# Optimization experiments

Measured on AMD Instinct MI355X. Metric: run time of the kernel, lower is better.

## Reference

```python
import jax, jax.numpy as jnp
import numpy as np

NUM_HEADS = 32
NUM_KV_HEADS = 8
HEAD_DIM = 128
SEQ = 2048
MASK_BLOCK = 128  # diffusion-LM denoising block size


def setup_inputs() -> dict:
    key = jax.random.key(0)
    kq, kk, kv = jax.random.split(key, 3)
    q = jax.random.normal(kq, (SEQ, NUM_HEADS * HEAD_DIM), dtype=jnp.float32)
    k = jax.random.normal(kk, (SEQ, NUM_KV_HEADS * HEAD_DIM), dtype=jnp.float32)
    v = jax.random.normal(kv, (SEQ, NUM_KV_HEADS * HEAD_DIM), dtype=jnp.float32)
    # block-causal mask at MASK_BLOCK granularity: token_q attends to token_kv
    # iff block(token_kv) <= block(token_q). Every row has >=1 True entry.
    blk = jnp.arange(SEQ) // MASK_BLOCK
    block_mask = blk[None, :] <= blk[:, None]  # [S, S] bool
    return {"q": q, "k": k, "v": v, "block_mask": block_mask}


def reference(q, k, v, block_mask):
    S = q.shape[0]
    scale = 1.0 / np.sqrt(HEAD_DIM).astype(np.float32)  # flex_attention default scale
    qh = q.reshape(S, NUM_HEADS, HEAD_DIM)       # [S, Hq, D]
    kh = k.reshape(S, NUM_KV_HEADS, HEAD_DIM)    # [S, Hkv, D]
    vh = v.reshape(S, NUM_KV_HEADS, HEAD_DIM)
    # GQA: repeat each kv head over its query-head group
    group = NUM_HEADS // NUM_KV_HEADS
    kh = jnp.repeat(kh, group, axis=1)           # [S, Hq, D]
    vh = jnp.repeat(vh, group, axis=1)
    scores = jnp.einsum('qhd,khd->hqk', qh, kh) * scale  # [Hq, S, S]
    neg_inf = jnp.finfo(scores.dtype).min
    scores = jnp.where(block_mask[None, :, :], scores, neg_inf)
    probs = jax.nn.softmax(scores, axis=-1)
    o = jnp.einsum('hqk,khd->qhd', probs, vh)    # [S, Hq, D]
    return o.reshape(S, NUM_HEADS * HEAD_DIM)
```

## Files before the change

### kernel.cpp

```cpp
#include <hip/hip_runtime.h>
#include <hip/hip_bf16.h>

#define SEQL  2048
#define NHQ   32
#define NHKV  8
#define HD    128

typedef __attribute__((ext_vector_type(4))) float          f32x4;
typedef __attribute__((ext_vector_type(8))) short          bf16x8;
typedef __attribute__((ext_vector_type(4))) unsigned short u16x4;
typedef __attribute__((ext_vector_type(8))) unsigned short u16x8;

__device__ __forceinline__ unsigned short f2bf(float f) {
  union { float f; unsigned u; } v; v.f = f;
  unsigned u = v.u;
  return (unsigned short)((u + 0x7fffu + ((u >> 16) & 1u)) >> 16);
}

__device__ __forceinline__ unsigned cvtpk_bf16(float lo, float hi) {
  unsigned r;
  asm("v_cvt_pk_bf16_f32 %0, %1, %2" : "=v"(r) : "v"(lo), "v"(hi));
  return r;
}

__device__ __forceinline__ void gload16(const void* g, void* l) {
  __builtin_amdgcn_global_load_lds(
      (const __attribute__((address_space(1))) unsigned int*)g,
      (__attribute__((address_space(3))) unsigned int*)l, 16, 0, 0);
}

__global__ __launch_bounds__(256) void prep_k(const float* __restrict__ k,
                                              unsigned short* __restrict__ kws) {
  int t = blockIdx.x * 256 + threadIdx.x;
  int s   = t >> 7;
  int col = (t & 127) << 3;
  int hkv = col >> 7;
  int d0  = col & 127;
  const float* src = k + (size_t)s * (NHKV * HD) + col;
  f32x4 a = *(const f32x4*)src;
  f32x4 b = *(const f32x4*)(src + 4);
  u16x8 r;
  r[0] = f2bf(a[0]); r[1] = f2bf(a[1]); r[2] = f2bf(a[2]); r[3] = f2bf(a[3]);
  r[4] = f2bf(b[0]); r[5] = f2bf(b[1]); r[6] = f2bf(b[2]); r[7] = f2bf(b[3]);
  int tile = s >> 6, rr = s & 63;
  int idx = (rr * 128 + d0) ^ ((rr & 7) << 3);
  *(u16x8*)(kws + (((size_t)(hkv * 32 + tile)) << 13) + idx) = r;
}

__global__ __launch_bounds__(256) void prep_v(const float* __restrict__ v,
                                              unsigned short* __restrict__ vws) {
  int t = blockIdx.x * 256 + threadIdx.x;
  int d    = t & 127;
  int hkv  = (t >> 7) & 7;
  int rest = t >> 10;
  int tile = rest >> 3;
  int g    = (rest >> 2) & 1;
  int lhi  = rest & 3;
  int s0   = tile * 64 + g * 32 + lhi * 4;
  const float* src = v + (size_t)s0 * (NHKV * HD) + hkv * HD + d;
  u16x8 r;
  #pragma unroll
  for (int j = 0; j < 8; ++j) {
    int soff = ((j >> 2) << 4) + (j & 3);
    r[j] = f2bf(src[(size_t)soff * (NHKV * HD)]);
  }
  int idx = (d * 64 + g * 32 + lhi * 8) ^ ((d & 7) << 3);
  *(u16x8*)(vws + (((size_t)(hkv * 32 + tile)) << 13) + idx) = r;
}

__global__ __launch_bounds__(256, 2) void attn_fwd12(
    const float* __restrict__ q,
    const unsigned short* __restrict__ kws,
    const unsigned short* __restrict__ vws,
    float* __restrict__ out)
{
  __shared__ unsigned short Kb[2][8192];
  __shared__ unsigned short Vb[2][8192];

  const int tid  = threadIdx.x;
  const int lane = tid & 63;
  const int wv   = tid >> 6;
  const int l15  = lane & 15;
  const int lhi  = lane >> 4;
  const int swzK = (l15 & 7) << 3;

  const int bx   = blockIdx.x;
  const int hkv  = bx & 7;
  const int h    = hkv * 4 + ((bx >> 3) & 3);
  const int idx2 = bx >> 5;
  const int pr   = (idx2 < 8) ? idx2 : (23 - idx2);
  const int qtA  = pr, qtB = 31 - pr;
  const int nA   = ((qtA >> 1) + 1) * 2;
  const int nB   = 34 - nA;

  const float qscale = 0.08838834764831845f * 1.4426950408889634f;
  const float THR = 11.5f;

  const unsigned short* ktiles = kws + (((size_t)hkv * 32) << 13);
  const unsigned short* vtiles = vws + (((size_t)hkv * 32) << 13);

  bf16x8 qfA[4], qfB[4];
  f32x4 oaccA[8], oaccB[8];
  float mrunA = -1e30f, lrunA = 0.f, mrunB = -1e30f, lrunB = 0.f;

  {
    const float* qbase = q + (size_t)(qtA * 64 + wv * 16 + l15) * (NHQ * HD) + h * HD + lhi * 8;
    #pragma unroll
    for (int c = 0; c < 4; ++c) {
      f32x4 a = *(const f32x4*)(qbase + c * 32);
      f32x4 b = *(const f32x4*)(qbase + c * 32 + 4);
      bf16x8 r;
      r[0] = (short)f2bf(a[0] * qscale);
      r[1] = (short)f2bf(a[1] * qscale);
      r[2] = (short)f2bf(a[2] * qscale);
      r[3] = (short)f2bf(a[3] * qscale);
      r[4] = (short)f2bf(b[0] * qscale);
      r[5] = (short)f2bf(b[1] * qscale);
      r[6] = (short)f2bf(b[2] * qscale);
      r[7] = (short)f2bf(b[3] * qscale);
      qfA[c] = r;
    }
  }
  {
    const float* qbase = q + (size_t)(qtB * 64 + wv * 16 + l15) * (NHQ * HD) + h * HD + lhi * 8;
    #pragma unroll
    for (int c = 0; c < 4; ++c) {
      f32x4 a = *(const f32x4*)(qbase + c * 32);
      f32x4 b = *(const f32x4*)(qbase + c * 32 + 4);
      bf16x8 r;
      r[0] = (short)f2bf(a[0] * qscale);
      r[1] = (short)f2bf(a[1] * qscale);
      r[2] = (short)f2bf(a[2] * qscale);
      r[3] = (short)f2bf(a[3] * qscale);
      r[4] = (short)f2bf(b[0] * qscale);
      r[5] = (short)f2bf(b[1] * qscale);
      r[6] = (short)f2bf(b[2] * qscale);
      r[7] = (short)f2bf(b[3] * qscale);
      qfB[c] = r;
    }
  }
  #pragma unroll
  for (int i = 0; i < 8; ++i) {
    oaccA[i] = (f32x4){0.f, 0.f, 0.f, 0.f};
    oaccB[i] = (f32x4){0.f, 0.f, 0.f, 0.f};
  }

  auto STAGE = [&](int b, int kvt) {
    const char* gk = (const char*)(ktiles + ((size_t)kvt << 13));
    const char* gv = (const char*)(vtiles + ((size_t)kvt << 13));
    char* lk = (char*)&Kb[b][0];
    char* lv = (char*)&Vb[b][0];
    #pragma unroll
    for (int i = 0; i < 4; ++i) {
      const int off = wv * 4096 + i * 1024;
      gload16(gk + off + lane * 16, lk + off);
      gload16(gv + off + lane * 16, lv + off);
    }
  };

  auto computeDual = [&](int b) {
    f32x4 saA[4], saB[4];
    __builtin_amdgcn_s_setprio(1);
    #pragma unroll
    for (int sub = 0; sub < 4; ++sub) {
      f32x4 aA = (f32x4){0.f, 0.f, 0.f, 0.f};
      f32x4 aB = (f32x4){0.f, 0.f, 0.f, 0.f};
      const int row = sub * 16 + l15;
      #pragma unroll
      for (int c = 0; c < 4; ++c) {
        bf16x8 kf = *(const bf16x8*)(&Kb[b][(row * 128 + c * 32 + lhi * 8) ^ swzK]);
        aA = __builtin_amdgcn_mfma_f32_16x16x32_bf16(kf, qfA[c], aA, 0, 0, 0);
        aB = __builtin_amdgcn_mfma_f32_16x16x32_bf16(kf, qfB[c], aB, 0, 0, 0);
      }
      saA[sub] = aA; saB[sub] = aB;
    }
    __builtin_amdgcn_s_setprio(0);
    float a0 = fmaxf(fmaxf(saA[0][0], saA[0][1]), fmaxf(saA[0][2], saA[0][3]));
    float a1 = fmaxf(fmaxf(saA[1][0], saA[1][1]), fmaxf(saA[1][2], saA[1][3]));
    float a2 = fmaxf(fmaxf(saA[2][0], saA[2][1]), fmaxf(saA[2][2], saA[2][3]));
    float a3 = fmaxf(fmaxf(saA[3][0], saA[3][1]), fmaxf(saA[3][2], saA[3][3]));
    float mtA = fmaxf(fmaxf(a0, a1), fmaxf(a2, a3));
    float b0 = fmaxf(fmaxf(saB[0][0], saB[0][1]), fmaxf(saB[0][2], saB[0][3]));
    float b1 = fmaxf(fmaxf(saB[1][0], saB[1][1]), fmaxf(saB[1][2], saB[1][3]));
    float b2 = fmaxf(fmaxf(saB[2][0], saB[2][1]), fmaxf(saB[2][2], saB[2][3]));
    float b3 = fmaxf(fmaxf(saB[3][0], saB[3][1]), fmaxf(saB[3][2], saB[3][3]));
    float mtB = fmaxf(fmaxf(b0, b1), fmaxf(b2, b3));
    mtA = fmaxf(mtA, __shfl_xor(mtA, 16));
    mtA = fmaxf(mtA, __shfl_xor(mtA, 32));
    mtB = fmaxf(mtB, __shfl_xor(mtB, 16));
    mtB = fmaxf(mtB, __shfl_xor(mtB, 32));
    int need = (mtA > mrunA + THR) || (mtB > mrunB + THR);
    if (__any(need)) {
      float mnA = fmaxf(mrunA, mtA), mnB = fmaxf(mrunB, mtB);
      float cA = exp2f(mrunA - mnA), cB = exp2f(mrunB - mnB);
      mrunA = mnA; mrunB = mnB;
      lrunA *= cA; lrunB *= cB;
      #pragma unroll
      for (int d = 0; d < 8; ++d) { oaccA[d] *= cA; oaccB[d] *= cB; }
    }
    unsigned pwA[8], pwB[8];
    {
      float ts = 0.f;
      #pragma unroll
      for (int sub = 0; sub < 4; ++sub) {
        float p0 = exp2f(saA[sub][0] - mrunA);
        float p1 = exp2f(saA[sub][1] - mrunA);
        float p2 = exp2f(saA[sub][2] - mrunA);
        float p3 = exp2f(saA[sub][3] - mrunA);
        ts += (p0 + p1) + (p2 + p3);
        pwA[2 * sub]     = cvtpk_bf16(p0, p1);
        pwA[2 * sub + 1] = cvtpk_bf16(p2, p3);
      }
      ts += __shfl_xor(ts, 16);
      ts += __shfl_xor(ts, 32);
      lrunA += ts;
    }
    {
      float ts = 0.f;
      #pragma unroll
      for (int sub = 0; sub < 4; ++sub) {
        float p0 = exp2f(saB[sub][0] - mrunB);
        float p1 = exp2f(saB[sub][1] - mrunB);
        float p2 = exp2f(saB[sub][2] - mrunB);
        float p3 = exp2f(saB[sub][3] - mrunB);
        ts += (p0 + p1) + (p2 + p3);
        pwB[2 * sub]     = cvtpk_bf16(p0, p1);
        pwB[2 * sub + 1] = cvtpk_bf16(p2, p3);
      }
      ts += __shfl_xor(ts, 16);
      ts += __shfl_xor(ts, 32);
      lrunB += ts;
    }
    __builtin_amdgcn_s_setprio(1);
    #pragma unroll
    for (int kc = 0; kc < 2; ++kc) {
      bf16x8 vr[8];
      #pragma unroll
      for (int dsub = 0; dsub < 8; ++dsub) {
        const int d = dsub * 16 + l15;
        vr[dsub] = *(const bf16x8*)(&Vb[b][(d * 64 + kc * 32 + lhi * 8) ^ swzK]);
      }
      union { unsigned u[4]; bf16x8 v8; } pA, pB;
      pA.u[0] = pwA[4 * kc + 0]; pA.u[1] = pwA[4 * kc + 1];
      pA.u[2] = pwA[4 * kc + 2]; pA.u[3] = pwA[4 * kc + 3];
      pB.u[0] = pwB[4 * kc + 0]; pB.u[1] = pwB[4 * kc + 1];
      pB.u[2] = pwB[4 * kc + 2]; pB.u[3] = pwB[4 * kc + 3];
      bf16x8 pfA = pA.v8, pfB = pB.v8;
      #pragma unroll
      for (int dsub = 0; dsub < 8; ++dsub) {
        oaccA[dsub] = __builtin_amdgcn_mfma_f32_16x16x32_bf16(vr[dsub], pfA, oaccA[dsub], 0, 0, 0);
        oaccB[dsub] = __builtin_amdgcn_mfma_f32_16x16x32_bf16(vr[dsub], pfB, oaccB[dsub], 0, 0, 0);
      }
    }
    __builtin_amdgcn_s_setprio(0);
  };

  auto computeB = [&](int b) {
    f32x4 sa[4];
    __builtin_amdgcn_s_setprio(1);
    #pragma unroll
    for (int sub = 0; sub < 4; ++sub) {
      f32x4 acc = (f32x4){0.f, 0.f, 0.f, 0.f};
      const int row = sub * 16 + l15;
      #pragma unroll
      for (int c = 0; c < 4; ++c) {
        bf16x8 kf = *(const bf16x8*)(&Kb[b][(row * 128 + c * 32 + lhi * 8) ^ swzK]);
        acc = __builtin_amdgcn_mfma_f32_16x16x32_bf16(kf, qfB[c], acc, 0, 0, 0);
      }
      sa[sub] = acc;
    }
    __builtin_amdgcn_s_setprio(0);
    bf16x8 vr[2][8];
    #pragma unroll
    for (int kc = 0; kc < 2; ++kc)
      #pragma unroll
      for (int dsub = 0; dsub < 8; ++dsub) {
        const int d = dsub * 16 + l15;
        vr[kc][dsub] = *(const bf16x8*)(&Vb[b][(d * 64 + kc * 32 + lhi * 8) ^ swzK]);
      }
    float m0 = fmaxf(fmaxf(sa[0][0], sa[0][1]), fmaxf(sa[0][2], sa[0][3]));
    float m1 = fmaxf(fmaxf(sa[1][0], sa[1][1]), fmaxf(sa[1][2], sa[1][3]));
    float m2 = fmaxf(fmaxf(sa[2][0], sa[2][1]), fmaxf(sa[2][2], sa[2][3]));
    float m3 = fmaxf(fmaxf(sa[3][0], sa[3][1]), fmaxf(sa[3][2], sa[3][3]));
    float mt = fmaxf(fmaxf(m0, m1), fmaxf(m2, m3));
    mt = fmaxf(mt, __shfl_xor(mt, 16));
    mt = fmaxf(mt, __shfl_xor(mt, 32));
    if (__any(mt > mrunB + THR)) {
      float mn = fmaxf(mrunB, mt);
      float c0 = exp2f(mrunB - mn);
      mrunB = mn; lrunB *= c0;
      #pragma unroll
      for (int d = 0; d < 8; ++d) oaccB[d] *= c0;
    }
    unsigned pw[8];
    {
      float ts = 0.f;
      #pragma unroll
      for (int sub = 0; sub < 4; ++sub) {
        float p0 = exp2f(sa[sub][0] - mrunB);
        float p1 = exp2f(sa[sub][1] - mrunB);
        float p2 = exp2f(sa[sub][2] - mrunB);
        float p3 = exp2f(sa[sub][3] - mrunB);
        ts += (p0 + p1) + (p2 + p3);
        pw[2 * sub]     = cvtpk_bf16(p0, p1);
        pw[2 * sub + 1] = cvtpk_bf16(p2, p3);
      }
      ts += __shfl_xor(ts, 16);
      ts += __shfl_xor(ts, 32);
      lrunB += ts;
    }
    __builtin_amdgcn_s_setprio(1);
    #pragma unroll
    for (int kc = 0; kc < 2; ++kc) {
      union { unsigned u[4]; bf16x8 v8; } pk;
      pk.u[0] = pw[4 * kc + 0];
      pk.u[1] = pw[4 * kc + 1];
      pk.u[2] = pw[4 * kc + 2];
      pk.u[3] = pw[4 * kc + 3];
      bf16x8 pf = pk.v8;
      #pragma unroll
      for (int dsub = 0; dsub < 8; ++dsub) {
        oaccB[dsub] = __builtin_amdgcn_mfma_f32_16x16x32_bf16(vr[kc][dsub], pf, oaccB[dsub], 0, 0, 0);
      }
    }
    __builtin_amdgcn_s_setprio(0);
  };

  STAGE(0, 0);
  int buf = 0;
  #pragma unroll 1
  for (int t = 0; t < nB; ++t) {
    if (t == nA) {
      float invl = 1.0f / lrunA;
      float* ob = out + (size_t)(qtA * 64 + wv * 16 + l15) * (NHQ * HD) + h * HD + lhi * 4;
      #pragma unroll
      for (int dsub = 0; dsub < 8; ++dsub)
        *(f32x4*)(ob + dsub * 16) = oaccA[dsub] * invl;
    }
    if (t + 1 < nB) {
      STAGE(buf ^ 1, t + 1);
      asm volatile("s_waitcnt vmcnt(8)" ::: "memory");
    } else {
      asm volatile("s_waitcnt vmcnt(0)" ::: "memory");
    }
    __builtin_amdgcn_s_barrier();
    asm volatile("" ::: "memory");
    if (t < nA) computeDual(buf);
    else        computeB(buf);
    asm volatile("" ::: "memory");
    __builtin_amdgcn_s_barrier();
    buf ^= 1;
  }
  {
    float invl = 1.0f / lrunB;
    float* ob = out + (size_t)(qtB * 64 + wv * 16 + l15) * (NHQ * HD) + h * HD + lhi * 4;
    #pragma unroll
    for (int dsub = 0; dsub < 8; ++dsub)
      *(f32x4*)(ob + dsub * 16) = oaccB[dsub] * invl;
  }
}

__global__ __launch_bounds__(256) void attn_v1(
    const float* __restrict__ q,
    const float* __restrict__ k,
    const float* __restrict__ v,
    float* __restrict__ out)
{
  __shared__ unsigned short Ks[64 * 128];
  __shared__ unsigned short Vt[128 * 64];
  __shared__ unsigned short Psl[4][16 * 64];

  const int tid  = threadIdx.x;
  const int lane = tid & 63;
  const int wv   = tid >> 6;
  const int bx   = blockIdx.x;
  const int h    = bx & 31;
  const int qt   = (SEQL / 64 - 1) - (bx >> 5);
  const int q0   = qt * 64;
  const int hkv  = h >> 2;
  const int l15 = lane & 15;
  const int lhi = lane >> 4;
  const float qscale = 0.08838834764831845f * 1.4426950408889634f;

  bf16x8 qf[4];
  {
    const float* qbase = q + (size_t)(q0 + wv * 16 + l15) * (NHQ * HD) + h * HD + lhi * 8;
    #pragma unroll
    for (int c = 0; c < 4; ++c) {
      const float* p8 = qbase + c * 32;
      f32x4 a = *(const f32x4*)p8;
      f32x4 b = *(const f32x4*)(p8 + 4);
      bf16x8 r;
      r[0] = (short)f2bf(a[0] * qscale); r[1] = (short)f2bf(a[1] * qscale);
      r[2] = (short)f2bf(a[2] * qscale); r[3] = (short)f2bf(a[3] * qscale);
      r[4] = (short)f2bf(b[0] * qscale); r[5] = (short)f2bf(b[1] * qscale);
      r[6] = (short)f2bf(b[2] * qscale); r[7] = (short)f2bf(b[3] * qscale);
      qf[c] = r;
    }
  }
  f32x4 oacc[8];
  #pragma unroll
  for (int i = 0; i < 8; ++i) oacc[i] = (f32x4){0.f, 0.f, 0.f, 0.f};
  float mrun[4], lrun[4];
  #pragma unroll
  for (int r = 0; r < 4; ++r) { mrun[r] = -1e30f; lrun[r] = 0.f; }
  const int ntiles = ((q0 >> 7) + 1) * 2;
  for (int t = 0; t < ntiles; ++t) {
    const int kv0 = t * 64;
    __syncthreads();
    #pragma unroll
    for (int it = 0; it < 8; ++it) {
      int c = it * 256 + tid;
      int row = c >> 5;
      int dc = (c & 31) << 2;
      f32x4 x = *(const f32x4*)(k + (size_t)(kv0 + row) * (NHKV * HD) + hkv * HD + dc);
      u16x4 y;
      y[0] = f2bf(x[0]); y[1] = f2bf(x[1]); y[2] = f2bf(x[2]); y[3] = f2bf(x[3]);
      int idx = (row * HD + dc) ^ ((row & 7) << 3);
      *(u16x4*)(&Ks[idx]) = y;
    }
    {
      int row = tid >> 2;
      int db = (tid & 3) << 5;
      const float* vbase = v + (size_t)(kv0 + row) * (NHKV * HD) + hkv * HD + db;
      #pragma unroll
      for (int it = 0; it < 8; ++it) {
        f32x4 x = *(const f32x4*)(vbase + it * 4);
        int d0 = db + it * 4;
        #pragma unroll
        for (int j = 0; j < 4; ++j) {
          int d = d0 + j;
          int idx = (d * 64 + row) ^ ((d & 7) << 3);
          Vt[idx] = f2bf(x[j]);
        }
      }
    }
    __syncthreads();
    f32x4 sacc[4];
    #pragma unroll
    for (int sub = 0; sub < 4; ++sub) {
      f32x4 acc = (f32x4){0.f, 0.f, 0.f, 0.f};
      #pragma unroll
      for (int c = 0; c < 4; ++c) {
        int row = sub * 16 + l15;
        int idx = (row * HD + c * 32 + lhi * 8) ^ ((row & 7) << 3);
        bf16x8 kf = *(const bf16x8*)(&Ks[idx]);
        acc = __builtin_amdgcn_mfma_f32_16x16x32_bf16(qf[c], kf, acc, 0, 0, 0);
      }
      sacc[sub] = acc;
    }
    float corr[4];
    #pragma unroll
    for (int r = 0; r < 4; ++r) {
      float mt = fmaxf(fmaxf(sacc[0][r], sacc[1][r]), fmaxf(sacc[2][r], sacc[3][r]));
      #pragma unroll
      for (int off = 1; off < 16; off <<= 1) mt = fmaxf(mt, __shfl_xor(mt, off));
      float mnew = fmaxf(mrun[r], mt);
      corr[r] = exp2f(mrun[r] - mnew);
      mrun[r] = mnew;
      float p0 = exp2f(sacc[0][r] - mnew);
      float p1 = exp2f(sacc[1][r] - mnew);
      float p2 = exp2f(sacc[2][r] - mnew);
      float p3 = exp2f(sacc[3][r] - mnew);
      int qr = (lhi << 2) + r;
      int swz = (qr & 7) << 3;
      int bq = qr * 64;
      Psl[wv][(bq + 0  + l15) ^ swz] = f2bf(p0);
      Psl[wv][(bq + 16 + l15) ^ swz] = f2bf(p1);
      Psl[wv][(bq + 32 + l15) ^ swz] = f2bf(p2);
      Psl[wv][(bq + 48 + l15) ^ swz] = f2bf(p3);
      float ts = p0 + p1 + p2 + p3;
      #pragma unroll
      for (int off = 1; off < 16; off <<= 1) ts += __shfl_xor(ts, off);
      lrun[r] = lrun[r] * corr[r] + ts;
    }
    #pragma unroll
    for (int dsub = 0; dsub < 8; ++dsub) {
      f32x4 o = oacc[dsub];
      o[0] *= corr[0]; o[1] *= corr[1]; o[2] *= corr[2]; o[3] *= corr[3];
      oacc[dsub] = o;
    }
    #pragma unroll
    for (int kc = 0; kc < 2; ++kc) {
      int pidx = (l15 * 64 + kc * 32 + lhi * 8) ^ ((l15 & 7) << 3);
      bf16x8 pf = *(const bf16x8*)(&Psl[wv][pidx]);
      #pragma unroll
      for (int dsub = 0; dsub < 8; ++dsub) {
        int d = dsub * 16 + l15;
        int vidx = (d * 64 + kc * 32 + lhi * 8) ^ ((d & 7) << 3);
        bf16x8 vf = *(const bf16x8*)(&Vt[vidx]);
        oacc[dsub] = __builtin_amdgcn_mfma_f32_16x16x32_bf16(pf, vf, oacc[dsub], 0, 0, 0);
      }
    }
  }
  float inv[4];
  #pragma unroll
  for (int r = 0; r < 4; ++r) inv[r] = 1.0f / lrun[r];
  float* obase = out + (size_t)(q0 + wv * 16 + (lhi << 2)) * (NHQ * HD) + h * HD + l15;
  #pragma unroll
  for (int dsub = 0; dsub < 8; ++dsub) {
    #pragma unroll
    for (int r = 0; r < 4; ++r) {
      obase[(size_t)r * (NHQ * HD) + dsub * 16] = oacc[dsub][r] * inv[r];
    }
  }
}

extern "C" void kernel_launch(void* const* d_in, const int* in_sizes, int n_in,
                              void* d_out, int out_size, void* d_ws, size_t ws_size,
                              hipStream_t stream) {
  const float* q = (const float*)d_in[0];
  const float* k = (const float*)d_in[1];
  const float* v = (const float*)d_in[2];
  float* out = (float*)d_out;
  const size_t prepNeed = (size_t)8 * 1024 * 1024 + 512;
  if (ws_size >= prepNeed) {
    unsigned short* kws = (unsigned short*)d_ws;
    unsigned short* vws = kws + (size_t)4 * 1024 * 1024 / 2;
    prep_k<<<1024, 256, 0, stream>>>(k, kws);
    prep_v<<<1024, 256, 0, stream>>>(v, vws);
    attn_fwd12<<<512, 256, 0, stream>>>(q, kws, vws, out);
  } else {
    attn_v1<<<1024, 256, 0, stream>>>(q, k, v, out);
  }
}
```

Measured before the change: 101.5 us.

## Split dual/single-tile attention loops and stream V fragments to cut register pressure

Splits the main loop into a dual-tile phase (tiles A and B together) and a B-only phase, removing the per-iteration branch and writing out A's result between the two loops. In the dual phase, the PV products for A and B are done one after the other, and V fragments are loaded from LDS inside the MFMA loop instead of holding 8 V registers and both P vectors at once. It also drops the minBlocks=2 launch bound. The aim is lower VGPR pressure and simpler control flow, at the cost of reading V from LDS twice per tile in the dual phase and possibly a different occupancy.

```diff
diff --git a/kernel.cpp b/kernel.cpp
--- a/kernel.cpp
+++ b/kernel.cpp
@@ -68,7 +68,7 @@
   *(u16x8*)(vws + (((size_t)(hkv * 32 + tile)) << 13) + idx) = r;
 }
 
-__global__ __launch_bounds__(256, 2) void attn_fwd12(
+__global__ __launch_bounds__(256) void attn_fwd13(
     const float* __restrict__ q,
     const unsigned short* __restrict__ kws,
     const unsigned short* __restrict__ vws,
@@ -99,12 +99,21 @@
   const unsigned short* ktiles = kws + (((size_t)hkv * 32) << 13);
   const unsigned short* vtiles = vws + (((size_t)hkv * 32) << 13);
 
-  bf16x8 qfA[4], qfB[4];
-  f32x4 oaccA[8], oaccB[8];
-  float mrunA = -1e30f, lrunA = 0.f, mrunB = -1e30f, lrunB = 0.f;
-
-  {
-    const float* qbase = q + (size_t)(qtA * 64 + wv * 16 + l15) * (NHQ * HD) + h * HD + lhi * 8;
+  auto STAGE = [&](int b, int kvt) {
+    const char* gk = (const char*)(ktiles + ((size_t)kvt << 13));
+    const char* gv = (const char*)(vtiles + ((size_t)kvt << 13));
+    char* lk = (char*)&Kb[b][0];
+    char* lv = (char*)&Vb[b][0];
+    #pragma unroll
+    for (int i = 0; i < 4; ++i) {
+      const int off = wv * 4096 + i * 1024;
+      gload16(gk + off + lane * 16, lk + off);
+      gload16(gv + off + lane * 16, lv + off);
+    }
+  };
+
+  auto loadQf = [&](int qt, bf16x8* qf) {
+    const float* qbase = q + (size_t)(qt * 64 + wv * 16 + l15) * (NHQ * HD) + h * HD + lhi * 8;
     #pragma unroll
     for (int c = 0; c < 4; ++c) {
       f32x4 a = *(const f32x4*)(qbase + c * 32);
@@ -118,225 +127,152 @@
       r[5] = (short)f2bf(b[1] * qscale);
       r[6] = (short)f2bf(b[2] * qscale);
       r[7] = (short)f2bf(b[3] * qscale);
-      qfA[c] = r;
-    }
-  }
-  {
-    const float* qbase = q + (size_t)(qtB * 64 + wv * 16 + l15) * (NHQ * HD) + h * HD + lhi * 8;
-    #pragma unroll
-    for (int c = 0; c < 4; ++c) {
-      f32x4 a = *(const f32x4*)(qbase + c * 32);
-      f32x4 b = *(const f32x4*)(qbase + c * 32 + 4);
-      bf16x8 r;
-      r[0] = (short)f2bf(a[0] * qscale);
-      r[1] = (short)f2bf(a[1] * qscale);
-      r[2] = (short)f2bf(a[2] * qscale);
-      r[3] = (short)f2bf(a[3] * qscale);
-      r[4] = (short)f2bf(b[0] * qscale);
-      r[5] = (short)f2bf(b[1] * qscale);
-      r[6] = (short)f2bf(b[2] * qscale);
-      r[7] = (short)f2bf(b[3] * qscale);
-      qfB[c] = r;
-    }
-  }
+      qf[c] = r;
+    }
+  };
+
+  bf16x8 qfA[4], qfB[4];
+  loadQf(qtA, qfA);
+  loadQf(qtB, qfB);
+
+  f32x4 oaccA[8], oaccB[8];
   #pragma unroll
   for (int i = 0; i < 8; ++i) {
     oaccA[i] = (f32x4){0.f, 0.f, 0.f, 0.f};
     oaccB[i] = (f32x4){0.f, 0.f, 0.f, 0.f};
   }
-
-  auto STAGE = [&](int b, int kvt) {
-    const char* gk = (const char*)(ktiles + ((size_t)kvt << 13));
-    const char* gv = (const char*)(vtiles + ((size_t)kvt << 13));
-    char* lk = (char*)&Kb[b][0];
-    char* lv = (char*)&Vb[b][0];
-    #pragma unroll
-    for (int i = 0; i < 4; ++i) {
-      const int off = wv * 4096 + i * 1024;
-      gload16(gk + off + lane * 16, lk + off);
-      gload16(gv + off + lane * 16, lv + off);
-    }
-  };
-
-  auto computeDual = [&](int b) {
-    f32x4 saA[4], saB[4];
-    __builtin_amdgcn_s_setprio(1);
-    #pragma unroll
-    for (int sub = 0; sub < 4; ++sub) {
-      f32x4 aA = (f32x4){0.f, 0.f, 0.f, 0.f};
-      f32x4 aB = (f32x4){0.f, 0.f, 0.f, 0.f};
-      const int row = sub * 16 + l15;
-      #pragma unroll
-      for (int c = 0; c < 4; ++c) {
-        bf16x8 kf = *(const bf16x8*)(&Kb[b][(row * 128 + c * 32 + lhi * 8) ^ swzK]);
-        aA = __builtin_amdgcn_mfma_f32_16x16x32_bf16(kf, qfA[c], aA, 0, 0, 0);
-        aB = __builtin_amdgcn_mfma_f32_16x16x32_bf16(kf, qfB[c], aB, 0, 0, 0);
-      }
-      saA[sub] = aA; saB[sub] = aB;
-    }
-    __builtin_amdgcn_s_setprio(0);
-    float a0 = fmaxf(fmaxf(saA[0][0], saA[0][1]), fmaxf(saA[0][2], saA[0][3]));
-    float a1 = fmaxf(fmaxf(saA[1][0], saA[1][1]), fmaxf(saA[1][2], saA[1][3]));
-    float a2 = fmaxf(fmaxf(saA[2][0], saA[2][1]), fmaxf(saA[2][2], saA[2][3]));
-    float a3 = fmaxf(fmaxf(saA[3][0], saA[3][1]), fmaxf(saA[3][2], saA[3][3]));
-    float mtA = fmaxf(fmaxf(a0, a1), fmaxf(a2, a3));
-    float b0 = fmaxf(fmaxf(saB[0][0], saB[0][1]), fmaxf(saB[0][2], saB[0][3]));
-    float b1 = fmaxf(fmaxf(saB[1][0], saB[1][1]), fmaxf(saB[1][2], saB[1][3]));
-    float b2 = fmaxf(fmaxf(saB[2][0], saB[2][1]), fmaxf(saB[2][2], saB[2][3]));
-    float b3 = fmaxf(fmaxf(saB[3][0], saB[3][1]), fmaxf(saB[3][2], saB[3][3]));
-    float mtB = fmaxf(fmaxf(b0, b1), fmaxf(b2, b3));
-    mtA = fmaxf(mtA, __shfl_xor(mtA, 16));
-    mtA = fmaxf(mtA, __shfl_xor(mtA, 32));
-    mtB = fmaxf(mtB, __shfl_xor(mtB, 16));
-    mtB = fmaxf(mtB, __shfl_xor(mtB, 32));
-    int need = (mtA > mrunA + THR) || (mtB > mrunB + THR);
-    if (__any(need)) {
-      float mnA = fmaxf(mrunA, mtA), mnB = fmaxf(mrunB, mtB);
-      float cA = exp2f(mrunA - mnA), cB = exp2f(mrunB - mnB);
-      mrunA = mnA; mrunB = mnB;
-      lrunA *= cA; lrunB *= cB;
-      #pragma unroll
-      for (int d = 0; d < 8; ++d) { oaccA[d] *= cA; oaccB[d] *= cB; }
-    }
-    unsigned pwA[8], pwB[8];
-    {
-      float ts = 0.f;
-      #pragma unroll
-      for (int sub = 0; sub < 4; ++sub) {
-        float p0 = exp2f(saA[sub][0] - mrunA);
-        float p1 = exp2f(saA[sub][1] - mrunA);
-        float p2 = exp2f(saA[sub][2] - mrunA);
-        float p3 = exp2f(saA[sub][3] - mrunA);
-        ts += (p0 + p1) + (p2 + p3);
-        pwA[2 * sub]     = cvtpk_bf16(p0, p1);
-        pwA[2 * sub + 1] = cvtpk_bf16(p2, p3);
-      }
-      ts += __shfl_xor(ts, 16);
-      ts += __shfl_xor(ts, 32);
-      lrunA += ts;
-    }
-    {
-      float ts = 0.f;
-      #pragma unroll
-      for (int sub = 0; sub < 4; ++sub) {
-        float p0 = exp2f(saB[sub][0] - mrunB);
-        float p1 = exp2f(saB[sub][1] - mrunB);
-        float p2 = exp2f(saB[sub][2] - mrunB);
-        float p3 = exp2f(saB[sub][3] - mrunB);
-        ts += (p0 + p1) + (p2 + p3);
-        pwB[2 * sub]     = cvtpk_bf16(p0, p1);
-        pwB[2 * sub + 1] = cvtpk_bf16(p2, p3);
-      }
-      ts += __shfl_xor(ts, 16);
-      ts += __shfl_xor(ts, 32);
-      lrunB += ts;
-    }
-    __builtin_amdgcn_s_setprio(1);
-    #pragma unroll
-    for (int kc = 0; kc < 2; ++kc) {
-      bf16x8 vr[8];
-      #pragma unroll
-      for (int dsub = 0; dsub < 8; ++dsub) {
-        const int d = dsub * 16 + l15;
-        vr[dsub] = *(const bf16x8*)(&Vb[b][(d * 64 + kc * 32 + lhi * 8) ^ swzK]);
-      }
-      union { unsigned u[4]; bf16x8 v8; } pA, pB;
-      pA.u[0] = pwA[4 * kc + 0]; pA.u[1] = pwA[4 * kc + 1];
-      pA.u[2] = pwA[4 * kc + 2]; pA.u[3] = pwA[4 * kc + 3];
-      pB.u[0] = pwB[4 * kc + 0]; pB.u[1] = pwB[4 * kc + 1];
-      pB.u[2] = pwB[4 * kc + 2]; pB.u[3] = pwB[4 * kc + 3];
-      bf16x8 pfA = pA.v8, pfB = pB.v8;
-      #pragma unroll
-      for (int dsub = 0; dsub < 8; ++dsub) {
-        oaccA[dsub] = __builtin_amdgcn_mfma_f32_16x16x32_bf16(vr[dsub], pfA, oaccA[dsub], 0, 0, 0);
-        oaccB[dsub] = __builtin_amdgcn_mfma_f32_16x16x32_bf16(vr[dsub], pfB, oaccB[dsub], 0, 0, 0);
-      }
-    }
-    __builtin_amdgcn_s_setprio(0);
-  };
-
-  auto computeB = [&](int b) {
-    f32x4 sa[4];
-    __builtin_amdgcn_s_setprio(1);
-    #pragma unroll
-    for (int sub = 0; sub < 4; ++sub) {
-      f32x4 acc = (f32x4){0.f, 0.f, 0.f, 0.f};
-      const int row = sub * 16 + l15;
-      #pragma unroll
-      for (int c = 0; c < 4; ++c) {
-        bf16x8 kf = *(const bf16x8*)(&Kb[b][(row * 128 + c * 32 + lhi * 8) ^ swzK]);
-        acc = __builtin_amdgcn_mfma_f32_16x16x32_bf16(kf, qfB[c], acc, 0, 0, 0);
-      }
-      sa[sub] = acc;
-    }
-    __builtin_amdgcn_s_setprio(0);
-    bf16x8 vr[2][8];
-    #pragma unroll
-    for (int kc = 0; kc < 2; ++kc)
-      #pragma unroll
-      for (int dsub = 0; dsub < 8; ++dsub) {
-        const int d = dsub * 16 + l15;
-        vr[kc][dsub] = *(const bf16x8*)(&Vb[b][(d * 64 + kc * 32 + lhi * 8) ^ swzK]);
-      }
-    float m0 = fmaxf(fmaxf(sa[0][0], sa[0][1]), fmaxf(sa[0][2], sa[0][3]));
-    float m1 = fmaxf(fmaxf(sa[1][0], sa[1][1]), fmaxf(sa[1][2], sa[1][3]));
-    float m2 = fmaxf(fmaxf(sa[2][0], sa[2][1]), fmaxf(sa[2][2], sa[2][3]));
-    float m3 = fmaxf(fmaxf(sa[3][0], sa[3][1]), fmaxf(sa[3][2], sa[3][3]));
-    float mt = fmaxf(fmaxf(m0, m1), fmaxf(m2, m3));
-    mt = fmaxf(mt, __shfl_xor(mt, 16));
-    mt = fmaxf(mt, __shfl_xor(mt, 32));
-    if (__any(mt > mrunB + THR)) {
-      float mn = fmaxf(mrunB, mt);
-      float c0 = exp2f(mrunB - mn);
-      mrunB = mn; lrunB *= c0;
-      #pragma unroll
-      for (int d = 0; d < 8; ++d) oaccB[d] *= c0;
-    }
-    unsigned pw[8];
-    {
-      float ts = 0.f;
-      #pragma unroll
-      for (int sub = 0; sub < 4; ++sub) {
-        float p0 = exp2f(sa[sub][0] - mrunB);
-        float p1 = exp2f(sa[sub][1] - mrunB);
-        float p2 = exp2f(sa[sub][2] - mrunB);
-        float p3 = exp2f(sa[sub][3] - mrunB);
-        ts += (p0 + p1) + (p2 + p3);
-        pw[2 * sub]     = cvtpk_bf16(p0, p1);
-        pw[2 * sub + 1] = cvtpk_bf16(p2, p3);
-      }
-      ts += __shfl_xor(ts, 16);
-      ts += __shfl_xor(ts, 32);
-      lrunB += ts;
-    }
-    __builtin_amdgcn_s_setprio(1);
-    #pragma unroll
-    for (int kc = 0; kc < 2; ++kc) {
-      union { unsigned u[4]; bf16x8 v8; } pk;
-      pk.u[0] = pw[4 * kc + 0];
-      pk.u[1] = pw[4 * kc + 1];
-      pk.u[2] = pw[4 * kc + 2];
-      pk.u[3] = pw[4 * kc + 3];
-      bf16x8 pf = pk.v8;
-      #pragma unroll
-      for (int dsub = 0; dsub < 8; ++dsub) {
-        oaccB[dsub] = __builtin_amdgcn_mfma_f32_16x16x32_bf16(vr[kc][dsub], pf, oaccB[dsub], 0, 0, 0);
-      }
-    }
-    __builtin_amdgcn_s_setprio(0);
-  };
+  float mrunA = -1e30f, lrunA = 0.f, mrunB = -1e30f, lrunB = 0.f;
 
   STAGE(0, 0);
   int buf = 0;
+
   #pragma unroll 1
-  for (int t = 0; t < nB; ++t) {
-    if (t == nA) {
-      float invl = 1.0f / lrunA;
-      float* ob = out + (size_t)(qtA * 64 + wv * 16 + l15) * (NHQ * HD) + h * HD + lhi * 4;
-      #pragma unroll
-      for (int dsub = 0; dsub < 8; ++dsub)
-        *(f32x4*)(ob + dsub * 16) = oaccA[dsub] * invl;
-    }
+  for (int t = 0; t < nA; ++t) {
+    STAGE(buf ^ 1, t + 1);
+    asm volatile("s_waitcnt vmcnt(8)" ::: "memory");
+    __builtin_amdgcn_s_barrier();
+    asm volatile("" ::: "memory");
+    {
+      const int b = buf;
+      f32x4 saA[4], saB[4];
+      __builtin_amdgcn_s_setprio(1);
+      #pragma unroll
+      for (int sub = 0; sub < 4; ++sub) {
+        f32x4 aA = (f32x4){0.f, 0.f, 0.f, 0.f};
+        f32x4 aB = (f32x4){0.f, 0.f, 0.f, 0.f};
+        const int row = sub * 16 + l15;
+        #pragma unroll
+        for (int c = 0; c < 4; ++c) {
+          bf16x8 kf = *(const bf16x8*)(&Kb[b][(row * 128 + c * 32 + lhi * 8) ^ swzK]);
+          aA = __builtin_amdgcn_mfma_f32_16x16x32_bf16(kf, qfA[c], aA, 0, 0, 0);
+          aB = __builtin_amdgcn_mfma_f32_16x16x32_bf16(kf, qfB[c], aB, 0, 0, 0);
+        }
+        saA[sub] = aA; saB[sub] = aB;
+      }
+      __builtin_amdgcn_s_setprio(0);
+      float a0 = fmaxf(fmaxf(saA[0][0], saA[0][1]), fmaxf(saA[0][2], saA[0][3]));
+      float a1 = fmaxf(fmaxf(saA[1][0], saA[1][1]), fmaxf(saA[1][2], saA[1][3]));
+      float a2 = fmaxf(fmaxf(saA[2][0], saA[2][1]), fmaxf(saA[2][2], saA[2][3]));
+      float a3 = fmaxf(fmaxf(saA[3][0], saA[3][1]), fmaxf(saA[3][2], saA[3][3]));
+      float mtA = fmaxf(fmaxf(a0, a1), fmaxf(a2, a3));
+      float b0 = fmaxf(fmaxf(saB[0][0], saB[0][1]), fmaxf(saB[0][2], saB[0][3]));
+      float b1 = fmaxf(fmaxf(saB[1][0], saB[1][1]), fmaxf(saB[1][2], saB[1][3]));
+      float b2 = fmaxf(fmaxf(saB[2][0], saB[2][1]), fmaxf(saB[2][2], saB[2][3]));
+      float b3 = fmaxf(fmaxf(saB[3][0], saB[3][1]), fmaxf(saB[3][2], saB[3][3]));
+      float mtB = fmaxf(fmaxf(b0, b1), fmaxf(b2, b3));
+      mtA = fmaxf(mtA, __shfl_xor(mtA, 16));
+      mtA = fmaxf(mtA, __shfl_xor(mtA, 32));
+      mtB = fmaxf(mtB, __shfl_xor(mtB, 16));
+      mtB = fmaxf(mtB, __shfl_xor(mtB, 32));
+      int need = (mtA > mrunA + THR) || (mtB > mrunB + THR);
+      if (__any(need)) {
+        float mnA = fmaxf(mrunA, mtA), mnB = fmaxf(mrunB, mtB);
+        float cA = exp2f(mrunA - mnA), cB = exp2f(mrunB - mnB);
+        mrunA = mnA; mrunB = mnB;
+        lrunA *= cA; lrunB *= cB;
+        #pragma unroll
+        for (int d = 0; d < 8; ++d) { oaccA[d] *= cA; oaccB[d] *= cB; }
+      }
+      {
+        unsigned pw[8];
+        float ts = 0.f;
+        #pragma unroll
+        for (int sub = 0; sub < 4; ++sub) {
+          float p0 = exp2f(saA[sub][0] - mrunA);
+          float p1 = exp2f(saA[sub][1] - mrunA);
+          float p2 = exp2f(saA[sub][2] - mrunA);
+          float p3 = exp2f(saA[sub][3] - mrunA);
+          ts += (p0 + p1) + (p2 + p3);
+          pw[2 * sub]     = cvtpk_bf16(p0, p1);
+          pw[2 * sub + 1] = cvtpk_bf16(p2, p3);
+        }
+        ts += __shfl_xor(ts, 16);
+        ts += __shfl_xor(ts, 32);
+        lrunA += ts;
+        __builtin_amdgcn_s_setprio(1);
+        #pragma unroll
+        for (int kc = 0; kc < 2; ++kc) {
+          union { unsigned u[4]; bf16x8 v8; } pk;
+          pk.u[0] = pw[4 * kc + 0]; pk.u[1] = pw[4 * kc + 1];
+          pk.u[2] = pw[4 * kc + 2]; pk.u[3] = pw[4 * kc + 3];
+          bf16x8 pf = pk.v8;
+          #pragma unroll
+          for (int dsub = 0; dsub < 8; ++dsub) {
+            const int d = dsub * 16 + l15;
+            bf16x8 vf = *(const bf16x8*)(&Vb[b][(d * 64 + kc * 32 + lhi * 8) ^ swzK]);
+            oaccA[dsub] = __builtin_amdgcn_mfma_f32_16x16x32_bf16(vf, pf, oaccA[dsub], 0, 0, 0);
+          }
+        }
+        __builtin_amdgcn_s_setprio(0);
+      }
+      {
+        unsigned pw[8];
+        float ts = 0.f;
+        #pragma unroll
+        for (int sub = 0; sub < 4; ++sub) {
+          float p0 = exp2f(saB[sub][0] - mrunB);
+          float p1 = exp2f(saB[sub][1] - mrunB);
+          float p2 = exp2f(saB[sub][2] - mrunB);
+          float p3 = exp2f(saB[sub][3] - mrunB);
+          ts += (p0 + p1) + (p2 + p3);
+          pw[2 * sub]     = cvtpk_bf16(p0, p1);
+          pw[2 * sub + 1] = cvtpk_bf16(p2, p3);
+        }
+        ts += __shfl_xor(ts, 16);
+        ts += __shfl_xor(ts, 32);
+        lrunB += ts;
+        __builtin_amdgcn_s_setprio(1);
+        #pragma unroll
+        for (int kc = 0; kc < 2; ++kc) {
+          union { unsigned u[4]; bf16x8 v8; } pk;
+          pk.u[0] = pw[4 * kc + 0]; pk.u[1] = pw[4 * kc + 1];
+          pk.u[2] = pw[4 * kc + 2]; pk.u[3] = pw[4 * kc + 3];
+          bf16x8 pf = pk.v8;
+          #pragma unroll
+          for (int dsub = 0; dsub < 8; ++dsub) {
+            const int d = dsub * 16 + l15;
+            bf16x8 vf = *(const bf16x8*)(&Vb[b][(d * 64 + kc * 32 + lhi * 8) ^ swzK]);
+            oaccB[dsub] = __builtin_amdgcn_mfma_f32_16x16x32_bf16(vf, pf, oaccB[dsub], 0, 0, 0);
+          }
+        }
+        __builtin_amdgcn_s_setprio(0);
+      }
+    }
+    asm volatile("" ::: "memory");
+    __builtin_amdgcn_s_barrier();
+    buf ^= 1;
+  }
+
+  {
+    float invl = 1.0f / lrunA;
+    float* ob = out + (size_t)(qtA * 64 + wv * 16 + l15) * (NHQ * HD) + h * HD + lhi * 4;
+    #pragma unroll
+    for (int dsub = 0; dsub < 8; ++dsub)
+      *(f32x4*)(ob + dsub * 16) = oaccA[dsub] * invl;
+  }
+
+  #pragma unroll 1
+  for (int t = nA; t < nB; ++t) {
     if (t + 1 < nB) {
       STAGE(buf ^ 1, t + 1);
       asm volatile("s_waitcnt vmcnt(8)" ::: "memory");
@@ -345,12 +281,82 @@
     }
     __builtin_amdgcn_s_barrier();
     asm volatile("" ::: "memory");
-    if (t < nA) computeDual(buf);
-    else        computeB(buf);
+    {
+      const int b = buf;
+      f32x4 sa[4];
+      __builtin_amdgcn_s_setprio(1);
+      #pragma unroll
+      for (int sub = 0; sub < 4; ++sub) {
+        f32x4 acc = (f32x4){0.f, 0.f, 0.f, 0.f};
+        const int row = sub * 16 + l15;
+        #pragma unroll
+        for (int c = 0; c < 4; ++c) {
+          bf16x8 kf = *(const bf16x8*)(&Kb[b][(row * 128 + c * 32 + lhi * 8) ^ swzK]);
+          acc = __builtin_amdgcn_mfma_f32_16x16x32_bf16(kf, qfB[c], acc, 0, 0, 0);
+        }
+        sa[sub] = acc;
+      }
+      __builtin_amdgcn_s_setprio(0);
+      bf16x8 vr[2][8];
+      #pragma unroll
+      for (int kc = 0; kc < 2; ++kc)
+        #pragma unroll
+        for (int dsub = 0; dsub < 8; ++dsub) {
+          const int d = dsub * 16 + l15;
+          vr[kc][dsub] = *(const bf16x8*)(&Vb[b][(d * 64 + kc * 32 + lhi * 8) ^ swzK]);
+        }
+      float m0 = fmaxf(fmaxf(sa[0][0], sa[0][1]), fmaxf(sa[0][2], sa[0][3]));
+      float m1 = fmaxf(fmaxf(sa[1][0], sa[1][1]), fmaxf(sa[1][2], sa[1][3]));
+      float m2 = fmaxf(fmaxf(sa[2][0], sa[2][1]), fmaxf(sa[2][2], sa[2][3]));
+      float m3 = fmaxf(fmaxf(sa[3][0], sa[3][1]), fmaxf(sa[3][2], sa[3][3]));
+      float mt = fmaxf(fmaxf(m0, m1), fmaxf(m2, m3));
+      mt = fmaxf(mt, __shfl_xor(mt, 16));
+      mt = fmaxf(mt, __shfl_xor(mt, 32));
+      if (__any(mt > mrunB + THR)) {
+        float mn = fmaxf(mrunB, mt);
+        float c0 = exp2f(mrunB - mn);
+        mrunB = mn; lrunB *= c0;
+        #pragma unroll
+        for (int d = 0; d < 8; ++d) oaccB[d] *= c0;
+      }
+      unsigned pw[8];
+      {
+        float ts = 0.f;
+        #pragma unroll
+        for (int sub = 0; sub < 4; ++sub) {
+          float p0 = exp2f(sa[sub][0] - mrunB);
+          float p1 = exp2f(sa[sub][1] - mrunB);
+          float p2 = exp2f(sa[sub][2] - mrunB);
+          float p3 = exp2f(sa[sub][3] - mrunB);
+          ts += (p0 + p1) + (p2 + p3);
+          pw[2 * sub]     = cvtpk_bf16(p0, p1);
+          pw[2 * sub + 1] = cvtpk_bf16(p2, p3);
+        }
+        ts += __shfl_xor(ts, 16);
+        ts += __shfl_xor(ts, 32);
+        lrunB += ts;
+      }
+      __builtin_amdgcn_s_setprio(1);
+      #pragma unroll
+      for (int kc = 0; kc < 2; ++kc) {
+        union { unsigned u[4]; bf16x8 v8; } pk;
+        pk.u[0] = pw[4 * kc + 0];
+        pk.u[1] = pw[4 * kc + 1];
+        pk.u[2] = pw[4 * kc + 2];
+        pk.u[3] = pw[4 * kc + 3];
+        bf16x8 pf = pk.v8;
+        #pragma unroll
+        for (int dsub = 0; dsub < 8; ++dsub) {
+          oaccB[dsub] = __builtin_amdgcn_mfma_f32_16x16x32_bf16(vr[kc][dsub], pf, oaccB[dsub], 0, 0, 0);
+        }
+      }
+      __builtin_amdgcn_s_setprio(0);
+    }
     asm volatile("" ::: "memory");
     __builtin_amdgcn_s_barrier();
     buf ^= 1;
   }
+
   {
     float invl = 1.0f / lrunB;
     float* ob = out + (size_t)(qtB * 64 + wv * 16 + l15) * (NHQ * HD) + h * HD + lhi * 4;
@@ -519,7 +525,7 @@
     unsigned short* vws = kws + (size_t)4 * 1024 * 1024 / 2;
     prep_k<<<1024, 256, 0, stream>>>(k, kws);
     prep_v<<<1024, 256, 0, stream>>>(v, vws);
-    attn_fwd12<<<512, 256, 0, stream>>>(q, kws, vws, out);
+    attn_fwd13<<<512, 256, 0, stream>>>(q, kws, vws, out);
   } else {
     attn_v1<<<1024, 256, 0, stream>>>(q, k, v, out);
   }
```

Result: slower. 121.5 us (+19.7%).
